# Performance work log

Hardware: AMD Instinct MI355X
Metric: run time of the kernel (lower is better)

## Reference

```python
import jax, jax.numpy as jnp
import numpy as np


def setup_inputs() -> dict:
    key = jax.random.key(0)
    kx, kf = jax.random.split(key)
    x = jax.random.normal(kx, (4, 8192, 1024), dtype=jnp.float32)
    filt = jax.random.normal(kf, (2048,), dtype=jnp.float32)
    return {"x": x, "filt": filt}


def reference(x, filt):
    # x: (batch, seq, dim); filt: (filter_length,)
    batch, seq, dim = x.shape
    L = filt.shape[0]
    pad = seq + L - 1
    # long-sequence FFT branch (seq > 64)
    xt = jnp.swapaxes(x, 1, 2)                 # (b, d, s)
    fx = jnp.fft.rfft(xt, n=pad, axis=-1)      # (b, d, pad//2+1) complex
    ff = jnp.fft.rfft(filt[::-1], n=pad)       # (pad//2+1,) complex
    conv = jnp.fft.irfft(fx * ff, n=pad, axis=-1)  # (b, d, pad)
    conv = conv[:, :, L - 1:L - 1 + seq]       # valid region, length seq
    return jnp.swapaxes(conv, 1, 2)            # (b, s, d)
```

## Files before the change

### kernel.cpp

```cpp
#include <hip/hip_runtime.h>

typedef unsigned short u16;
typedef unsigned int   u32;

#define BATCH 4
#define SEQ   8192
#define DIM   1024
#define FL    2048
#define TROW  10240

#define BM 256
#define BN 64
#define BK 64
#define NSTAGE 36
#define WOFF 64
#define NW   2272
#define WIN_HI 2110

typedef float  f32x4  __attribute__((ext_vector_type(4)));
typedef __bf16 bf16x8 __attribute__((ext_vector_type(8)));
typedef short  s16x8  __attribute__((ext_vector_type(8)));

typedef const __attribute__((address_space(1))) void* gas_t;
typedef __attribute__((address_space(3))) void* las_t;

__device__ __forceinline__ u16 f2bf(float f) {
  u32 u = __float_as_uint(f);
  u += 0x7fffu + ((u >> 16) & 1u);
  return (u16)(u >> 16);
}

__global__ __launch_bounds__(256) void k_transpose(const float* __restrict__ x,
                                                   u16* __restrict__ xT) {
  __shared__ __align__(16) u16 sm[64 * 66];
  const int bid = blockIdx.x;
  const int tb = bid % (TROW / 64);
  const int db = (bid / (TROW / 64)) % (DIM / 64);
  const int b  = bid / ((TROW / 64) * (DIM / 64));
  const int t0 = tb * 64, d0 = db * 64;
  const int tid = threadIdx.x;

  const int c4 = tid & 15;
  const int lt = tid >> 4;
  const float* xb = x + (size_t)b * SEQ * DIM + d0 + c4 * 4;
  #pragma unroll
  for (int s = 0; s < 64; s += 16) {
    const int tl = lt + s;
    const int t = t0 + tl;
    float4 v = make_float4(0.f, 0.f, 0.f, 0.f);
    if (t < SEQ) v = *(const float4*)(xb + (size_t)t * DIM);
    u32 p0 = (u32)f2bf(v.x) | ((u32)f2bf(v.y) << 16);
    u32 p1 = (u32)f2bf(v.z) | ((u32)f2bf(v.w) << 16);
    u32* dst = (u32*)&sm[tl * 66 + c4 * 4];
    dst[0] = p0;
    dst[1] = p1;
  }
  __syncthreads();
  const int q  = tid & 7;
  const int dl = tid >> 3;
  u16* xo = xT + ((size_t)b * DIM + d0) * TROW + t0 + 8 * q;
  #pragma unroll
  for (int s = 0; s < 2; ++s) {
    const int d = dl + 32 * s;
    u32 w[4];
    #pragma unroll
    for (int h = 0; h < 4; ++h) {
      w[h] = (u32)sm[(8 * q + 2 * h) * 66 + d] |
             ((u32)sm[(8 * q + 2 * h + 1) * 66 + d] << 16);
    }
    *(uint4*)(xo + (size_t)d * TROW) = *(const uint4*)w;
  }
}

__global__ __launch_bounds__(256, 3) void k_conv(const u16* __restrict__ xT,
                                                 const float* __restrict__ filt,
                                                 float* __restrict__ out) {
  __shared__ __align__(16) u16 Wb[NW * 8];
  __shared__ __align__(16) u16 Xs[2][BN * BK];

  const int bid = blockIdx.x;
  const int tb = bid & 31;
  const int db = (bid >> 5) & 15;
  const int b  = bid >> 9;
  const int t0 = tb * BM;
  const int d0 = db * BN;

  const int tid  = threadIdx.x;
  const int wid  = tid >> 6;
  const int lane = tid & 63;
  const int quad = lane >> 4;
  const int lq   = lane & 15;
  const int Tw   = wid * 64;

  const u16* xrow = xT + ((size_t)b * DIM + d0) * TROW + t0;
  const int p0 = wid * 128 + lane;
  const int p1 = p0 + 64;
  const int ds0 = p0 >> 3, kc0 = (p0 & 7) ^ (ds0 & 7);
  const int ds1 = p1 >> 3, kc1 = (p1 & 7) ^ (ds1 & 7);
  const u16* gp0 = xrow + (size_t)ds0 * TROW + kc0 * 8;
  const u16* gp1 = xrow + (size_t)ds1 * TROW + kc1 * 8;

  {
    u16* nb = &Xs[0][wid * 1024];
    __builtin_amdgcn_global_load_lds((gas_t)gp0, (las_t)nb, 16, 0, 0);
    __builtin_amdgcn_global_load_lds((gas_t)gp1, (las_t)(nb + 512), 16, 0, 0);
  }

  for (int w = tid; w < NW; w += 256) {
    const int base = w - WOFF;
    u32 pk[4];
    #pragma unroll
    for (int h = 0; h < 4; ++h) {
      const int i0 = base + 2 * h;
      const int i1 = i0 + 1;
      const float v0 = (i0 >= 0 && i0 < FL) ? filt[i0] : 0.f;
      const float v1 = (i1 >= 0 && i1 < FL) ? filt[i1] : 0.f;
      pk[h] = (u32)f2bf(v0) | ((u32)f2bf(v1) << 16);
    }
    u32* dst = (u32*)&Wb[w * 8];
    dst[0] = pk[0]; dst[1] = pk[1]; dst[2] = pk[2]; dst[3] = pk[3];
  }

  f32x4 acc[4][4];
  const f32x4 fz = {0.f, 0.f, 0.f, 0.f};
  #pragma unroll
  for (int i = 0; i < 4; ++i)
    #pragma unroll
    for (int j = 0; j < 4; ++j) acc[i][j] = fz;

  const s16x8 sz = {0, 0, 0, 0, 0, 0, 0, 0};
  bf16x8 roll0 = __builtin_bit_cast(bf16x8, sz);
  bf16x8 roll1 = roll0;

  const int wconst = quad * 8 - Tw - lq + WOFF;
  const int kkLo = Tw - 31;
  const int kkHi = Tw + WIN_HI;

  for (int st = 0; st < NSTAGE; ++st) {
    __syncthreads();
    if (st + 1 < NSTAGE) {
      const int kkn = (st + 1) * BK;
      u16* nb = &Xs[(st + 1) & 1][wid * 1024];
      __builtin_amdgcn_global_load_lds((gas_t)(gp0 + kkn), (las_t)nb, 16, 0, 0);
      __builtin_amdgcn_global_load_lds((gas_t)(gp1 + kkn), (las_t)(nb + 512), 16, 0, 0);
    }
    const u16* Xc = &Xs[st & 1][0];
    const int kk0 = st * BK;
    #pragma unroll
    for (int half = 0; half < 2; ++half) {
      const int kk = kk0 + half * 32;
      if (kk >= kkLo && kk <= kkHi) {
        bf16x8 bfr[4];
        #pragma unroll
        for (int nt = 0; nt < 4; ++nt) {
          const int dl = nt * 16 + lq;
          const int kc = (half * 4 + quad) ^ (dl & 7);
          bfr[nt] = *(const bf16x8*)&Xc[(dl * 8 + kc) * 8];
        }
        const int w0 = kk + wconst;
        const bf16x8 a0 = *(const bf16x8*)&Wb[w0 * 8];
        const bf16x8 a1 = *(const bf16x8*)&Wb[(w0 - 16) * 8];
        __builtin_amdgcn_s_setprio(1);
        #pragma unroll
        for (int nt = 0; nt < 4; ++nt) {
          acc[0][nt] = __builtin_amdgcn_mfma_f32_16x16x32_bf16(a0,    bfr[nt], acc[0][nt], 0, 0, 0);
          acc[1][nt] = __builtin_amdgcn_mfma_f32_16x16x32_bf16(a1,    bfr[nt], acc[1][nt], 0, 0, 0);
          acc[2][nt] = __builtin_amdgcn_mfma_f32_16x16x32_bf16(roll0, bfr[nt], acc[2][nt], 0, 0, 0);
          acc[3][nt] = __builtin_amdgcn_mfma_f32_16x16x32_bf16(roll1, bfr[nt], acc[3][nt], 0, 0, 0);
        }
        __builtin_amdgcn_s_setprio(0);
        roll0 = a0; roll1 = a1;
      }
    }
  }

  float* ob = out + ((size_t)b * SEQ + t0 + Tw) * DIM + d0;
  #pragma unroll
  for (int mt = 0; mt < 4; ++mt) {
    #pragma unroll
    for (int nt = 0; nt < 4; ++nt) {
      #pragma unroll
      for (int r = 0; r < 4; ++r) {
        ob[(size_t)(mt * 16 + quad * 4 + r) * DIM + nt * 16 + lq] = acc[mt][nt][r];
      }
    }
  }
}

extern "C" void kernel_launch(void* const* d_in, const int* in_sizes, int n_in,
                              void* d_out, int out_size, void* d_ws, size_t ws_size,
                              hipStream_t stream) {
  const float* x    = (const float*)d_in[0];
  const float* filt = (const float*)d_in[1];
  float* out = (float*)d_out;
  u16* xT = (u16*)d_ws;
  (void)in_sizes; (void)n_in; (void)out_size; (void)ws_size;

  k_transpose<<<BATCH * (TROW / 64) * (DIM / 64), 256, 0, stream>>>(x, xT);
  k_conv<<<BATCH * 32 * 16, 256, 0, stream>>>(xT, filt, out);
}
```

Measured before the change: 349.2 us.

## Deepen X tile pipeline to four LDS buffers with three-ahead async prefetch

Halves the K step to 32 and doubles the stage count. It replaces the double buffer with a 4-slot ring in which each wave issues its direct-to-LDS load three stages ahead. Each stage now waits with explicit vmcnt counters plus a raw s_barrier instead of a full __syncthreads, which keeps more global loads in flight and hides memory latency. The cost is a barrier per 32-wide step instead of per 64, and the vmcnt bookkeeping is fragile if the compiler emits other memory operations.

```diff
diff --git a/kernel.cpp b/kernel.cpp
--- a/kernel.cpp
+++ b/kernel.cpp
@@ -11,8 +11,9 @@
 
 #define BM 256
 #define BN 64
-#define BK 64
-#define NSTAGE 36
+#define BK 32
+#define NSTAGE 72
+#define NBUF 4
 #define WOFF 64
 #define NW   2272
 #define WIN_HI 2110
@@ -76,7 +77,7 @@
                                                  const float* __restrict__ filt,
                                                  float* __restrict__ out) {
   __shared__ __align__(16) u16 Wb[NW * 8];
-  __shared__ __align__(16) u16 Xs[2][BN * BK];
+  __shared__ __align__(16) u16 Xs[NBUF][BN * BK];
 
   const int bid = blockIdx.x;
   const int tb = bid & 31;
@@ -93,17 +94,14 @@
   const int Tw   = wid * 64;
 
   const u16* xrow = xT + ((size_t)b * DIM + d0) * TROW + t0;
-  const int p0 = wid * 128 + lane;
-  const int p1 = p0 + 64;
-  const int ds0 = p0 >> 3, kc0 = (p0 & 7) ^ (ds0 & 7);
-  const int ds1 = p1 >> 3, kc1 = (p1 & 7) ^ (ds1 & 7);
+  const int p0 = wid * 64 + lane;
+  const int ds0 = p0 >> 2, kc0 = (p0 & 3) ^ ((ds0 >> 1) & 3);
   const u16* gp0 = xrow + (size_t)ds0 * TROW + kc0 * 8;
-  const u16* gp1 = xrow + (size_t)ds1 * TROW + kc1 * 8;
-
-  {
-    u16* nb = &Xs[0][wid * 1024];
-    __builtin_amdgcn_global_load_lds((gas_t)gp0, (las_t)nb, 16, 0, 0);
-    __builtin_amdgcn_global_load_lds((gas_t)gp1, (las_t)(nb + 512), 16, 0, 0);
+
+  #pragma unroll
+  for (int p = 0; p < 3; ++p) {
+    __builtin_amdgcn_global_load_lds((gas_t)(gp0 + p * BK),
+                                     (las_t)&Xs[p][wid * 512], 16, 0, 0);
   }
 
   for (int w = tid; w < NW; w += 256) {
@@ -137,40 +135,45 @@
   const int kkHi = Tw + WIN_HI;
 
   for (int st = 0; st < NSTAGE; ++st) {
-    __syncthreads();
-    if (st + 1 < NSTAGE) {
-      const int kkn = (st + 1) * BK;
-      u16* nb = &Xs[(st + 1) & 1][wid * 1024];
-      __builtin_amdgcn_global_load_lds((gas_t)(gp0 + kkn), (las_t)nb, 16, 0, 0);
-      __builtin_amdgcn_global_load_lds((gas_t)(gp1 + kkn), (las_t)(nb + 512), 16, 0, 0);
-    }
-    const u16* Xc = &Xs[st & 1][0];
-    const int kk0 = st * BK;
-    #pragma unroll
-    for (int half = 0; half < 2; ++half) {
-      const int kk = kk0 + half * 32;
-      if (kk >= kkLo && kk <= kkHi) {
-        bf16x8 bfr[4];
-        #pragma unroll
-        for (int nt = 0; nt < 4; ++nt) {
-          const int dl = nt * 16 + lq;
-          const int kc = (half * 4 + quad) ^ (dl & 7);
-          bfr[nt] = *(const bf16x8*)&Xc[(dl * 8 + kc) * 8];
-        }
-        const int w0 = kk + wconst;
-        const bf16x8 a0 = *(const bf16x8*)&Wb[w0 * 8];
-        const bf16x8 a1 = *(const bf16x8*)&Wb[(w0 - 16) * 8];
-        __builtin_amdgcn_s_setprio(1);
-        #pragma unroll
-        for (int nt = 0; nt < 4; ++nt) {
-          acc[0][nt] = __builtin_amdgcn_mfma_f32_16x16x32_bf16(a0,    bfr[nt], acc[0][nt], 0, 0, 0);
-          acc[1][nt] = __builtin_amdgcn_mfma_f32_16x16x32_bf16(a1,    bfr[nt], acc[1][nt], 0, 0, 0);
-          acc[2][nt] = __builtin_amdgcn_mfma_f32_16x16x32_bf16(roll0, bfr[nt], acc[2][nt], 0, 0, 0);
-          acc[3][nt] = __builtin_amdgcn_mfma_f32_16x16x32_bf16(roll1, bfr[nt], acc[3][nt], 0, 0, 0);
-        }
-        __builtin_amdgcn_s_setprio(0);
-        roll0 = a0; roll1 = a1;
+    if (st == 0) {
+      __syncthreads();
+    } else {
+      __builtin_amdgcn_sched_barrier(0);
+      if (st + 2 < NSTAGE)      asm volatile("s_waitcnt vmcnt(2)");
+      else if (st + 1 < NSTAGE) asm volatile("s_waitcnt vmcnt(1)");
+      else                      asm volatile("s_waitcnt vmcnt(0)");
+      __builtin_amdgcn_sched_barrier(0);
+      __builtin_amdgcn_s_barrier();
+      __builtin_amdgcn_sched_barrier(0);
+    }
+    if (st + 3 < NSTAGE) {
+      __builtin_amdgcn_global_load_lds((gas_t)(gp0 + (st + 3) * BK),
+                                       (las_t)&Xs[(st + 3) & (NBUF - 1)][wid * 512],
+                                       16, 0, 0);
+    }
+    const int kk = st * BK;
+    if (kk >= kkLo && kk <= kkHi) {
+      const u16* Xc = &Xs[st & (NBUF - 1)][0];
+      bf16x8 bfr[4];
+      #pragma unroll
+      for (int nt = 0; nt < 4; ++nt) {
+        const int dl = nt * 16 + lq;
+        const int kc = quad ^ ((dl >> 1) & 3);
+        bfr[nt] = *(const bf16x8*)&Xc[(dl * 4 + kc) * 8];
       }
+      const int w0 = kk + wconst;
+      const bf16x8 a0 = *(const bf16x8*)&Wb[w0 * 8];
+      const bf16x8 a1 = *(const bf16x8*)&Wb[(w0 - 16) * 8];
+      __builtin_amdgcn_s_setprio(1);
+      #pragma unroll
+      for (int nt = 0; nt < 4; ++nt) {
+        acc[0][nt] = __builtin_amdgcn_mfma_f32_16x16x32_bf16(a0,    bfr[nt], acc[0][nt], 0, 0, 0);
+        acc[1][nt] = __builtin_amdgcn_mfma_f32_16x16x32_bf16(a1,    bfr[nt], acc[1][nt], 0, 0, 0);
+        acc[2][nt] = __builtin_amdgcn_mfma_f32_16x16x32_bf16(roll0, bfr[nt], acc[2][nt], 0, 0, 0);
+        acc[3][nt] = __builtin_amdgcn_mfma_f32_16x16x32_bf16(roll1, bfr[nt], acc[3][nt], 0, 0, 0);
+      }
+      __builtin_amdgcn_s_setprio(0);
+      roll0 = a0; roll1 = a1;
     }
   }
 
```

Result: slower. 361.0 us (+3.4%).
